# Performance work log

Measured on AMD Instinct MI355X. Metric: run time of the kernel, lower is better.

The kernel has to match this reference:

```python
import jax, jax.numpy as jnp
import numpy as np

P = 32            # patch_num_row
KS = 5            # kernel_size
DIM = 1024
HEADS = 16
DIM_HEAD = 64
INNER = HEADS * DIM_HEAD
SCALE = DIM_HEAD ** -0.5


def _nearby_mask(p=P, ks=KS):
    # True = masked out (matches torch masked_fill semantics)
    pad = ks // 2
    m = np.ones((p * p, p + 2 * pad, p + 2 * pad), dtype=bool)
    for i in range(p):
        for j in range(p):
            m[i * p + j, i:i + ks, j:j + ks] = False
    m = m[:, pad:-pad, pad:-pad].reshape(p * p, p * p)
    # F.pad(mask, (1,0,1,0), value=False): unmasked first row/col (BOS token)
    m = np.pad(m, ((1, 0), (1, 0)), constant_values=False)
    return jnp.asarray(m)  # [n, n], n = p*p + 1

NB_MASK = _nearby_mask()


def setup_inputs() -> dict:
    key = jax.random.key(0)
    ks = jax.random.split(key, 8)
    b, n = 16, P * P + 1
    s = DIM ** -0.5
    return {
        "q": jax.random.normal(ks[0], (b, n, DIM), jnp.float32),
        "k": jax.random.normal(ks[1], (b, n, DIM), jnp.float32),
        "v": jax.random.normal(ks[2], (b, n, DIM), jnp.float32),
        "Wq": jax.random.normal(ks[3], (DIM, INNER), jnp.float32) * s,
        "Wk": jax.random.normal(ks[4], (DIM, INNER), jnp.float32) * s,
        "Wv": jax.random.normal(ks[5], (DIM, INNER), jnp.float32) * s,
        "Wo": jax.random.normal(ks[6], (INNER, DIM), jnp.float32) * (INNER ** -0.5),
        "bo": jnp.zeros((DIM,), jnp.float32),
    }


def reference(q, k, v, Wq, Wk, Wv, Wo, bo):
    b, n, _ = q.shape
    h, d = HEADS, DIM_HEAD
    # projections, split heads: b n (h d) -> b h n d
    qh = (q @ Wq).reshape(b, n, h, d).transpose(0, 2, 1, 3)
    kh = (k @ Wk).reshape(b, n, h, d).transpose(0, 2, 1, 3)
    vh = (v @ Wv).reshape(b, n, h, d).transpose(0, 2, 1, 3)
    dots = jnp.einsum('bhid,bhjd->bhij', qh, kh) * SCALE
    mask_value = -jnp.finfo(dots.dtype).max
    dots = jnp.where(NB_MASK[None, None], mask_value, dots)
    attn = jax.nn.softmax(dots, axis=-1)
    out = jnp.einsum('bhij,bhjd->bhid', attn, vh)
    out = out.transpose(0, 2, 1, 3).reshape(b, n, h * d)
    return out @ Wo + bo
```

## Files before the change

### kernel.cpp

```cpp
#include <hip/hip_runtime.h>

typedef unsigned short u16;
typedef unsigned int   u32;
typedef __attribute__((ext_vector_type(8))) __bf16 bf16x8;
typedef __attribute__((ext_vector_type(4))) float   f32x4;

#define MROWS 16400
#define NPADROWS 16512
#define KD 1024
#define MATEL ((size_t)NPADROWS * KD)
#define NT 32

__device__ __forceinline__ u16 f2b(float f) {
  union { float f; u32 u; } x; x.f = f;
  return (u16)((x.u + 0x7FFFu + ((x.u >> 16) & 1u)) >> 16);
}
__device__ __forceinline__ float b2f(u16 h) {
  union { u32 u; float f; } x; x.u = ((u32)h) << 16;
  return x.f;
}

__device__ __forceinline__ void gll16(const u16* g, u16* l) {
  __builtin_amdgcn_global_load_lds(
      (const __attribute__((address_space(1))) void*)g,
      (__attribute__((address_space(3))) void*)l, 16, 0, 0);
}

__global__ __launch_bounds__(256) void k_pre(
    const float* __restrict__ W0, const float* __restrict__ W1,
    const float* __restrict__ W2, const float* __restrict__ W3,
    u16* __restrict__ T,
    const float* __restrict__ q, const float* __restrict__ k,
    const float* __restrict__ v, u16* __restrict__ dst)
{
  if (blockIdx.x < 4096) {
    __shared__ float tile[32][33];
    int z = blockIdx.x >> 10;
    int tl = blockIdx.x & 1023;
    int k0 = (tl >> 5) * 32, n0 = (tl & 31) * 32;
    int tx = threadIdx.x & 31, ty = threadIdx.x >> 5;
    const float* W = (z == 0) ? W0 : (z == 1) ? W1 : (z == 2) ? W2 : W3;
    u16* Tz = T + (size_t)z * KD * KD;
#pragma unroll
    for (int r = ty; r < 32; r += 8)
      tile[r][tx] = W[(size_t)(k0 + r) * KD + n0 + tx];
    __syncthreads();
#pragma unroll
    for (int r = ty; r < 32; r += 8)
      Tz[(size_t)(n0 + r) * KD + k0 + tx] = f2b(tile[tx][r]);
  } else {
    int cid = blockIdx.x - 4096;
    const size_t CH_PER_MAT = MATEL / 8;
    const size_t total = 3 * CH_PER_MAT;
    for (size_t c = (size_t)cid * 256 + threadIdx.x; c < total;
         c += (size_t)2048 * 256) {
      size_t z = c / CH_PER_MAT;
      size_t r = c - z * CH_PER_MAT;
      size_t row = r >> 7;
      int col8 = (int)(r & 127) * 8;
      u16* o = dst + z * MATEL + row * KD + col8;
      if (row < MROWS) {
        const float* s = ((z == 0) ? q : (z == 1) ? k : v) + row * KD + col8;
        float4 f0 = *(const float4*)s;
        float4 f1 = *(const float4*)(s + 4);
        ushort4 o0; o0.x = f2b(f0.x); o0.y = f2b(f0.y); o0.z = f2b(f0.z); o0.w = f2b(f0.w);
        ushort4 o1; o1.x = f2b(f1.x); o1.y = f2b(f1.y); o1.z = f2b(f1.z); o1.w = f2b(f1.w);
        *(ushort4*)o = o0; *(ushort4*)(o + 4) = o1;
      } else {
        ushort4 zz; zz.x = zz.y = zz.z = zz.w = 0;
        *(ushort4*)o = zz; *(ushort4*)(o + 4) = zz;
      }
    }
  }
}

template<bool OUT_FP32>
__global__ __launch_bounds__(512, 1) void k_gemm256(
    const u16* __restrict__ Ab, const u16* __restrict__ Bt,
    u16* __restrict__ Cb, float* __restrict__ Cf,
    const float* __restrict__ bias, int nwg)
{
  __shared__ u16 lds[3 * 16384];

  int lin = blockIdx.x;
  int qq = nwg >> 3, r8 = nwg & 7;
  int xcd = lin & 7, pos = lin >> 3;
  int wg = (xcd < r8 ? xcd * (qq + 1) : r8 * (qq + 1) + (xcd - r8) * qq) + pos;
  int bn = wg & 3;
  int rest = wg >> 2;
  int bm = rest % 65;
  int z  = rest / 65;

  int t = threadIdx.x;
  int w = t >> 6, l = t & 63;
  int lrow = l & 15, kgrp = l >> 4;
  int wrow = w >> 2, wcol = w & 3;

  int pr = t >> 2;
  int ccl = ((t & 3) ^ ((t >> 3) & 3)) * 8;
  int ar0 = bm * 256 + pr;        if (ar0 > NPADROWS - 1) ar0 = NPADROWS - 1;
  int ar1 = bm * 256 + 128 + pr;  if (ar1 > NPADROWS - 1) ar1 = NPADROWS - 1;
  const u16* gA0 = Ab + (size_t)z * MATEL + (size_t)ar0 * KD + ccl;
  const u16* gA1 = Ab + (size_t)z * MATEL + (size_t)ar1 * KD + ccl;
  const u16* gB0 = Bt + (size_t)z * (1024 * 1024) + (size_t)(bn * 256 + pr) * KD + ccl;
  const u16* gB1 = gB0 + (size_t)128 * KD;

  int qr = (lrow >> 1) & 3;
  int xk = (kgrp ^ qr) * 8;

  f32x4 acc[8][4] = {};
  bf16x8 afr[4], bfr2[2];

#define STAGE(B) { u16* L = lds + (B) * 16384;                          \
    gll16(gA0, L + w * 512);          gll16(gA1, L + 4096 + w * 512);   \
    gll16(gB0, L + 8192 + w * 512);   gll16(gB1, L + 12288 + w * 512);  \
    gA0 += 32; gA1 += 32; gB0 += 32; gB1 += 32; }

#define WAITV4 do { __builtin_amdgcn_sched_barrier(0);                  \
    asm volatile("s_waitcnt vmcnt(4)" ::: "memory");                    \
    __builtin_amdgcn_sched_barrier(0); } while (0)
#define WAITV0 do { __builtin_amdgcn_sched_barrier(0);                  \
    asm volatile("s_waitcnt vmcnt(0)" ::: "memory");                    \
    __builtin_amdgcn_sched_barrier(0); } while (0)
#define BAR do { __builtin_amdgcn_sched_barrier(0);                     \
    __builtin_amdgcn_s_barrier();                                       \
    __builtin_amdgcn_sched_barrier(0); } while (0)

#define READ_A(FM0) {                                                   \
    _Pragma("unroll")                                                   \
    for (int qa = 0; qa < 4; ++qa)                                      \
      afr[qa] = *(const bf16x8*)(Lb + (wrow * 128 + (FM0 + qa) * 16 + lrow) * 32 + xk); }
#define READ_B(FN0) {                                                   \
    _Pragma("unroll")                                                   \
    for (int qb = 0; qb < 2; ++qb)                                      \
      bfr2[qb] = *(const bf16x8*)(Lb + 8192 + (wcol * 64 + (FN0 + qb) * 16 + lrow) * 32 + xk); }
#define MFMA_Q(FM0, FN0) {                                              \
    __builtin_amdgcn_s_setprio(1);                                      \
    _Pragma("unroll")                                                   \
    for (int qa = 0; qa < 4; ++qa)                                      \
      _Pragma("unroll")                                                 \
      for (int qb = 0; qb < 2; ++qb)                                    \
        acc[FM0 + qa][FN0 + qb] = __builtin_amdgcn_mfma_f32_16x16x32_bf16( \
            afr[qa], bfr2[qb], acc[FM0 + qa][FN0 + qb], 0, 0, 0);       \
    __builtin_amdgcn_s_setprio(0); }

  STAGE(0); STAGE(1);
  WAITV4;
  BAR;

  int cur = 0;
  for (int kt = 0; kt < NT; ++kt) {
    if (kt + 2 < NT) {
      int pre = cur + 2; if (pre >= 3) pre -= 3;
      STAGE(pre);
    }
    const u16* Lb = lds + cur * 16384;
    READ_A(0); READ_B(0);
    BAR; MFMA_Q(0, 0); BAR;
    READ_B(2);
    BAR; MFMA_Q(0, 2); BAR;
    READ_A(4);
    BAR; MFMA_Q(4, 2); BAR;
    READ_B(0);
    BAR; MFMA_Q(4, 0);
    if (kt + 1 < NT) {
      if (kt + 2 < NT) { WAITV4; }
      else            { WAITV0; }
      BAR;
    }
    cur += 1; if (cur == 3) cur = 0;
  }
#undef STAGE
#undef WAITV4
#undef WAITV0
#undef BAR
#undef READ_A
#undef READ_B
#undef MFMA_Q

#pragma unroll
  for (int fm = 0; fm < 8; ++fm) {
#pragma unroll
    for (int fn = 0; fn < 4; ++fn) {
      int gcol = bn * 256 + wcol * 64 + fn * 16 + lrow;
#pragma unroll
      for (int r = 0; r < 4; ++r) {
        int grow = bm * 256 + wrow * 128 + fm * 16 + kgrp * 4 + r;
        if constexpr (OUT_FP32) {
          if (grow < MROWS)
            Cf[(size_t)grow * KD + gcol] = acc[fm][fn][r] + bias[gcol];
        } else {
          if (grow < NPADROWS)
            Cb[(size_t)z * MATEL + (size_t)grow * KD + gcol] = f2b(acc[fm][fn][r]);
        }
      }
    }
  }
}

template<bool OUT_FP32>
__global__ __launch_bounds__(256) void k_gemm(
    const u16* __restrict__ Ab, const u16* __restrict__ Bt,
    u16* __restrict__ Cb, float* __restrict__ Cf,
    const float* __restrict__ bias, int nwg)
{
  __shared__ u16 lds[2 * 8192];

  int lin = blockIdx.x;
  int cpx = nwg >> 3;
  int swz = (lin & 7) * cpx + (lin >> 3);
  int bn = swz & 7;
  int rest = swz >> 3;
  int bm = rest % 129;
  int z  = rest / 129;

  int t = threadIdx.x;
  int w = t >> 6, l = t & 63;
  int lrow = l & 15, kgrp = l >> 4;
  int wm = (w >> 1) * 64, wn = (w & 1) * 64;

  int srow = w * 16 + (l >> 2);
  int scol = ((l & 3) ^ ((srow >> 1) & 3)) * 8;
  const u16* gA  = Ab + (size_t)z * MATEL + (size_t)(bm * 128 + srow) * KD + scol;
  const u16* gA2 = gA + (size_t)64 * KD;
  const u16* gB  = Bt + (size_t)z * (1024 * 1024) + (size_t)(bn * 128 + srow) * KD + scol;
  const u16* gB2 = gB + (size_t)64 * KD;
  int dA0 = w * 512;
  int dA1 = 2048 + w * 512;
  int dB0 = 4096 + w * 512;
  int dB1 = 6144 + w * 512;

  int qr = (lrow >> 1) & 3;
  int aoff[4], boff[4];
#pragma unroll
  for (int fm = 0; fm < 4; ++fm)
    aoff[fm] = (wm + fm * 16 + lrow) * 32 + ((kgrp ^ qr) * 8);
#pragma unroll
  for (int fn = 0; fn < 4; ++fn)
    boff[fn] = 4096 + (wn + fn * 16 + lrow) * 32 + ((kgrp ^ qr) * 8);

  f32x4 acc[4][4] = {};

#define STAGE(B) { u16* L = lds + (B) * 8192;                         \
    gll16(gA,  L + dA0); gll16(gA2, L + dA1);                         \
    gll16(gB,  L + dB0); gll16(gB2, L + dB1);                         \
    gA += 32; gA2 += 32; gB += 32; gB2 += 32; }

  STAGE(0);
  __syncthreads();

  int buf = 0;
#pragma unroll 2
  for (int kt = 0; kt < NT; ++kt) {
    if (kt + 1 < NT) STAGE(buf ^ 1);

    const u16* Lb = lds + buf * 8192;
    bf16x8 af[4], bfr[4];
#pragma unroll
    for (int fm = 0; fm < 4; ++fm)
      af[fm] = *(const bf16x8*)(Lb + aoff[fm]);
#pragma unroll
    for (int fn = 0; fn < 4; ++fn)
      bfr[fn] = *(const bf16x8*)(Lb + boff[fn]);
#pragma unroll
    for (int fm = 0; fm < 4; ++fm)
#pragma unroll
      for (int fn = 0; fn < 4; ++fn)
        acc[fm][fn] = __builtin_amdgcn_mfma_f32_16x16x32_bf16(af[fm], bfr[fn], acc[fm][fn], 0, 0, 0);

    __syncthreads();
    buf ^= 1;
  }
#undef STAGE

#pragma unroll
  for (int fm = 0; fm < 4; ++fm) {
#pragma unroll
    for (int fn = 0; fn < 4; ++fn) {
      int gcol = bn * 128 + wn + fn * 16 + lrow;
#pragma unroll
      for (int r = 0; r < 4; ++r) {
        int grow = bm * 128 + wm + fm * 16 + kgrp * 4 + r;
        if constexpr (OUT_FP32) {
          if (grow < MROWS)
            Cf[(size_t)grow * KD + gcol] = acc[fm][fn][r] + bias[gcol];
        } else {
          Cb[(size_t)z * MATEL + (size_t)grow * KD + gcol] = f2b(acc[fm][fn][r]);
        }
      }
    }
  }
}

__global__ __launch_bounds__(256) void k_attn(
    const u16* __restrict__ Qp, const u16* __restrict__ Kp,
    const u16* __restrict__ Vp, u16* __restrict__ AO)
{
  int t = threadIdx.x;

  if (blockIdx.x >= 256) {
    __shared__ float sdp[4][16][37];
    __shared__ int   keys[37];
    __shared__ unsigned long long incm[4];

    int bid = blockIdx.x - 256;
    int b = bid >> 8;
    int tile = bid & 255;
    int pi0 = (tile >> 4) * 2, pj0 = (tile & 15) * 2;
    size_t rowbase = (size_t)b * 1025;

    int iq[4];
#pragma unroll
    for (int qi = 0; qi < 4; ++qi)
      iq[qi] = 1 + (pi0 + (qi >> 1)) * 32 + (pj0 + (qi & 1));

    if (t < 37) {
      if (t < 36) {
        int r = pi0 - 2 + t / 6, c = pj0 - 2 + t % 6;
        keys[t] = (r >= 0 && r < 32 && c >= 0 && c < 32) ? (1 + r * 32 + c) : -1;
      } else {
        keys[36] = 0;
      }
    }
    if (t < 4) {
      int di = t >> 1, dj = t & 1;
      unsigned long long m = 1ull << 36;
      for (int j = 0; j < 36; ++j) {
        int wr = j / 6, wc = j % 6;
        if (wr >= di && wr < di + 5 && wc >= dj && wc < dj + 5) m |= 1ull << j;
      }
      incm[t] = m;
    }

    int e = t & 3;
    int hD = (t >> 2) & 15;
    float qreg[4][16];
#pragma unroll
    for (int qi = 0; qi < 4; ++qi) {
      const u16* qp = Qp + (rowbase + iq[qi]) * 1024 + hD * 64 + e * 16;
      uint4 a0 = *(const uint4*)qp;
      uint4 a1 = *(const uint4*)(qp + 8);
      u32 uu[8] = {a0.x, a0.y, a0.z, a0.w, a1.x, a1.y, a1.z, a1.w};
#pragma unroll
      for (int u = 0; u < 8; ++u) {
        qreg[qi][u * 2]     = __uint_as_float(uu[u] << 16);
        qreg[qi][u * 2 + 1] = __uint_as_float(uu[u] & 0xffff0000u);
      }
    }
    __syncthreads();

#pragma unroll
    for (int p = 0; p < 10; ++p) {
      int idx = p * 64 + (t >> 2);
      int j = idx >> 4; if (j > 36) j = 36;
      int key = keys[j];
      int krow = key < 0 ? 0 : key;
      const u16* kp = Kp + (rowbase + krow) * 1024 + hD * 64 + e * 16;
      uint4 kv0 = *(const uint4*)kp;
      uint4 kv1 = *(const uint4*)(kp + 8);
      float s0 = 0.f, s1 = 0.f, s2 = 0.f, s3 = 0.f;
      u32 uu[8] = {kv0.x, kv0.y, kv0.z, kv0.w, kv1.x, kv1.y, kv1.z, kv1.w};
#pragma unroll
      for (int u = 0; u < 8; ++u) {
        float lo = __uint_as_float(uu[u] << 16);
        float hi = __uint_as_float(uu[u] & 0xffff0000u);
        s0 += qreg[0][u * 2] * lo + qreg[0][u * 2 + 1] * hi;
        s1 += qreg[1][u * 2] * lo + qreg[1][u * 2 + 1] * hi;
        s2 += qreg[2][u * 2] * lo + qreg[2][u * 2 + 1] * hi;
        s3 += qreg[3][u * 2] * lo + qreg[3][u * 2 + 1] * hi;
      }
      s0 += __shfl_xor(s0, 1); s0 += __shfl_xor(s0, 2);
      s1 += __shfl_xor(s1, 1); s1 += __shfl_xor(s1, 2);
      s2 += __shfl_xor(s2, 1); s2 += __shfl_xor(s2, 2);
      s3 += __shfl_xor(s3, 1); s3 += __shfl_xor(s3, 2);
      if (idx < 592) {
        float sv = (e == 0) ? s0 : (e == 1) ? s1 : (e == 2) ? s2 : s3;
        sdp[e][hD][j] = (key >= 0) ? sv * 0.125f : -3.0e38f;
      }
    }
    __syncthreads();

    {
      int row = t >> 2;
      int qi = row >> 4, hh = row & 15;
      unsigned long long inc = incm[qi];
      float dv[10];
      float m = -3.0e38f;
#pragma unroll
      for (int s = 0; s < 10; ++s) {
        int j = e + s * 4;
        float d = -3.0e38f;
        if (j < 37) {
          d = sdp[qi][hh][j];
          if (!((inc >> j) & 1)) d = -3.0e38f;
        }
        dv[s] = d;
        m = fmaxf(m, d);
      }
      m = fmaxf(m, __shfl_xor(m, 1));
      m = fmaxf(m, __shfl_xor(m, 2));
      float sum = 0.f;
      float pv[10];
#pragma unroll
      for (int s = 0; s < 10; ++s) {
        int j = e + s * 4;
        float p = (j < 37) ? __expf(dv[s] - m) : 0.f;
        pv[s] = p; sum += p;
      }
      sum += __shfl_xor(sum, 1);
      sum += __shfl_xor(sum, 2);
      float inv = 1.f / sum;
#pragma unroll
      for (int s = 0; s < 10; ++s) {
        int j = e + s * 4;
        if (j < 37) sdp[qi][hh][j] = pv[s] * inv;
      }
    }
    __syncthreads();

    {
      int h = t >> 4;
      int c0 = t * 4;
      float a[4][4] = {};
#pragma unroll 4
      for (int j = 0; j < 37; ++j) {
        int key = keys[j];
        int krow = key < 0 ? 0 : key;
        ushort4 vv = *(const ushort4*)(Vp + (rowbase + krow) * 1024 + c0);
        float v0 = b2f(vv.x), v1 = b2f(vv.y), v2 = b2f(vv.z), v3 = b2f(vv.w);
#pragma unroll
        for (int qi = 0; qi < 4; ++qi) {
          float p = sdp[qi][h][j];
          a[qi][0] += p * v0; a[qi][1] += p * v1;
          a[qi][2] += p * v2; a[qi][3] += p * v3;
        }
      }
#pragma unroll
      for (int qi = 0; qi < 4; ++qi) {
        ushort4 o;
        o.x = f2b(a[qi][0]); o.y = f2b(a[qi][1]);
        o.z = f2b(a[qi][2]); o.w = f2b(a[qi][3]);
        *(ushort4*)&AO[(rowbase + iq[qi]) * 1024 + c0] = o;
      }
    }
  } else {
    __shared__ float q0[64];
    __shared__ float pr[1025];
    __shared__ float red[256];
    __shared__ float red4[256][4];
    int bid = blockIdx.x;
    int b = bid >> 4, h = bid & 15;
    size_t rowbase = (size_t)b * 1025;

    if (t < 64) q0[t] = b2f(Qp[rowbase * 1024 + h * 64 + t]);
    __syncthreads();

    float lmax = -3.0e38f;
    for (int j = t; j < 1025; j += 256) {
      const u16* kp = Kp + (rowbase + j) * 1024 + h * 64;
      float s = 0.f;
#pragma unroll
      for (int e = 0; e < 64; e += 4) {
        ushort4 kv = *(const ushort4*)(kp + e);
        s += q0[e + 0] * b2f(kv.x) + q0[e + 1] * b2f(kv.y)
           + q0[e + 2] * b2f(kv.z) + q0[e + 3] * b2f(kv.w);
      }
      s *= 0.125f;
      pr[j] = s;
      lmax = fmaxf(lmax, s);
    }
    red[t] = lmax; __syncthreads();
    for (int s = 128; s > 0; s >>= 1) {
      if (t < s) red[t] = fmaxf(red[t], red[t + s]);
      __syncthreads();
    }
    float m = red[0]; __syncthreads();

    float lsum = 0.f;
    for (int j = t; j < 1025; j += 256) {
      float p = __expf(pr[j] - m);
      pr[j] = p; lsum += p;
    }
    red[t] = lsum; __syncthreads();
    for (int s = 128; s > 0; s >>= 1) {
      if (t < s) red[t] += red[t + s];
      __syncthreads();
    }
    float inv = 1.f / red[0]; __syncthreads();

    int g16 = t & 15, grp = t >> 4;
    int c0 = h * 64 + g16 * 4;
    float a0 = 0, a1 = 0, a2 = 0, a3 = 0;
    for (int j = grp; j < 1025; j += 16) {
      float p = pr[j];
      ushort4 vv = *(const ushort4*)(Vp + (rowbase + j) * 1024 + c0);
      a0 += p * b2f(vv.x); a1 += p * b2f(vv.y);
      a2 += p * b2f(vv.z); a3 += p * b2f(vv.w);
    }
    red4[t][0] = a0; red4[t][1] = a1; red4[t][2] = a2; red4[t][3] = a3;
    __syncthreads();
    for (int s = 128; s >= 16; s >>= 1) {
      if (t < s) {
#pragma unroll
        for (int kx = 0; kx < 4; ++kx) red4[t][kx] += red4[t + s][kx];
      }
      __syncthreads();
    }
    if (t < 16) {
      ushort4 o;
      o.x = f2b(red4[t][0] * inv); o.y = f2b(red4[t][1] * inv);
      o.z = f2b(red4[t][2] * inv); o.w = f2b(red4[t][3] * inv);
      *(ushort4*)&AO[rowbase * 1024 + h * 64 + t * 4] = o;
    }
  }
}

extern "C" void kernel_launch(void* const* d_in, const int* in_sizes, int n_in,
                              void* d_out, int out_size, void* d_ws, size_t ws_size,
                              hipStream_t stream) {
  const float* q  = (const float*)d_in[0];
  const float* k  = (const float*)d_in[1];
  const float* v  = (const float*)d_in[2];
  const float* Wq = (const float*)d_in[3];
  const float* Wk = (const float*)d_in[4];
  const float* Wv = (const float*)d_in[5];
  const float* Wo = (const float*)d_in[6];
  const float* bo = (const float*)d_in[7];
  float* out = (float*)d_out;

  u16* wt = (u16*)d_ws;
  u16* qb = wt + (size_t)4 * 1024 * 1024;
  u16* Qp = qb + 3 * MATEL;
  u16* Kp = Qp + MATEL;
  u16* Vp = Kp + MATEL;
  u16* AO = qb;

  k_pre<<<6144, 256, 0, stream>>>(Wq, Wk, Wv, Wo, wt, q, k, v, qb);

  k_gemm256<false><<<780, 512, 0, stream>>>(qb, wt, Qp, nullptr, nullptr, 780);

  k_attn<<<4352, 256, 0, stream>>>(Qp, Kp, Vp, AO);

  k_gemm<true><<<1032, 256, 0, stream>>>(AO, wt + (size_t)3 * 1024 * 1024,
                                         nullptr, out, bo, 1032);
}
```

Baseline: 350.0 us.

## Compute local-window QK scores with MFMA and fuse masked softmax in registers

In the neighbourhood-attention blocks, the scalar per-thread QK dot product is replaced by bf16 16x16x32 MFMA instructions. Each wave handles four heads against 48 padded key slots, and Q/K fragments are loaded straight from global memory. The masked softmax now runs on the MFMA accumulators using cross-lane shuffles, and the normalized probabilities go to shared memory. This removes the separate score and softmax phases and one barrier. In exchange, the 16-row MFMA tile holds only 4 distinct queries, so most of its work is redundant.

```diff
diff --git a/kernel.cpp b/kernel.cpp
--- a/kernel.cpp
+++ b/kernel.cpp
@@ -2,6 +2,7 @@
 
 typedef unsigned short u16;
 typedef unsigned int   u32;
+typedef unsigned long long u64;
 typedef __attribute__((ext_vector_type(8))) __bf16 bf16x8;
 typedef __attribute__((ext_vector_type(4))) float   f32x4;
 
@@ -301,7 +302,7 @@
   if (blockIdx.x >= 256) {
     __shared__ float sdp[4][16][37];
     __shared__ int   keys[37];
-    __shared__ unsigned long long incm[4];
+    __shared__ u64   incm[4];
 
     int bid = blockIdx.x - 256;
     int b = bid >> 8;
@@ -324,96 +325,95 @@
     }
     if (t < 4) {
       int di = t >> 1, dj = t & 1;
-      unsigned long long m = 1ull << 36;
+      u64 m = 1ull << 36;
       for (int j = 0; j < 36; ++j) {
         int wr = j / 6, wc = j % 6;
         if (wr >= di && wr < di + 5 && wc >= dj && wc < dj + 5) m |= 1ull << j;
       }
       incm[t] = m;
     }
-
-    int e = t & 3;
-    int hD = (t >> 2) & 15;
-    float qreg[4][16];
-#pragma unroll
-    for (int qi = 0; qi < 4; ++qi) {
-      const u16* qp = Qp + (rowbase + iq[qi]) * 1024 + hD * 64 + e * 16;
-      uint4 a0 = *(const uint4*)qp;
-      uint4 a1 = *(const uint4*)(qp + 8);
-      u32 uu[8] = {a0.x, a0.y, a0.z, a0.w, a1.x, a1.y, a1.z, a1.w};
-#pragma unroll
-      for (int u = 0; u < 8; ++u) {
-        qreg[qi][u * 2]     = __uint_as_float(uu[u] << 16);
-        qreg[qi][u * 2 + 1] = __uint_as_float(uu[u] & 0xffff0000u);
-      }
-    }
     __syncthreads();
 
-#pragma unroll
-    for (int p = 0; p < 10; ++p) {
-      int idx = p * 64 + (t >> 2);
-      int j = idx >> 4; if (j > 36) j = 36;
-      int key = keys[j];
-      int krow = key < 0 ? 0 : key;
-      const u16* kp = Kp + (rowbase + krow) * 1024 + hD * 64 + e * 16;
-      uint4 kv0 = *(const uint4*)kp;
-      uint4 kv1 = *(const uint4*)(kp + 8);
-      float s0 = 0.f, s1 = 0.f, s2 = 0.f, s3 = 0.f;
-      u32 uu[8] = {kv0.x, kv0.y, kv0.z, kv0.w, kv1.x, kv1.y, kv1.z, kv1.w};
-#pragma unroll
-      for (int u = 0; u < 8; ++u) {
-        float lo = __uint_as_float(uu[u] << 16);
-        float hi = __uint_as_float(uu[u] & 0xffff0000u);
-        s0 += qreg[0][u * 2] * lo + qreg[0][u * 2 + 1] * hi;
-        s1 += qreg[1][u * 2] * lo + qreg[1][u * 2 + 1] * hi;
-        s2 += qreg[2][u * 2] * lo + qreg[2][u * 2 + 1] * hi;
-        s3 += qreg[3][u * 2] * lo + qreg[3][u * 2 + 1] * hi;
-      }
-      s0 += __shfl_xor(s0, 1); s0 += __shfl_xor(s0, 2);
-      s1 += __shfl_xor(s1, 1); s1 += __shfl_xor(s1, 2);
-      s2 += __shfl_xor(s2, 1); s2 += __shfl_xor(s2, 2);
-      s3 += __shfl_xor(s3, 1); s3 += __shfl_xor(s3, 2);
-      if (idx < 592) {
-        float sv = (e == 0) ? s0 : (e == 1) ? s1 : (e == 2) ? s2 : s3;
-        sdp[e][hD][j] = (key >= 0) ? sv * 0.125f : -3.0e38f;
-      }
-    }
-    __syncthreads();
-
     {
-      int row = t >> 2;
-      int qi = row >> 4, hh = row & 15;
-      unsigned long long inc = incm[qi];
-      float dv[10];
-      float m = -3.0e38f;
-#pragma unroll
-      for (int s = 0; s < 10; ++s) {
-        int j = e + s * 4;
-        float d = -3.0e38f;
-        if (j < 37) {
-          d = sdp[qi][hh][j];
-          if (!((inc >> j) & 1)) d = -3.0e38f;
+      int l = t & 63, w = t >> 6;
+      int kap = l & 15, kg = l >> 4;
+
+      int jj0 = kap, jj1 = 16 + kap, jj2 = 32 + kap;
+      int kraw0 = keys[jj0];
+      int kraw1 = keys[jj1];
+      int kraw2 = (jj2 < 37) ? keys[jj2] : -1;
+      int krow0 = kraw0 < 0 ? 0 : kraw0;
+      int krow1 = kraw1 < 0 ? 0 : kraw1;
+      int krow2 = kraw2 < 0 ? 0 : kraw2;
+      int qrow = iq[kap & 3];
+
+      u64 im0 = incm[0], im1 = incm[1], im2 = incm[2], im3 = incm[3];
+
+      const float NEG = -3.0e38f;
+      const size_t qoff = (rowbase + qrow) * 1024 + kg * 8;
+      const size_t k0off = (rowbase + krow0) * 1024 + kg * 8;
+      const size_t k1off = (rowbase + krow1) * 1024 + kg * 8;
+      const size_t k2off = (rowbase + krow2) * 1024 + kg * 8;
+
+#pragma unroll
+      for (int hh = 0; hh < 4; ++hh) {
+        int h = w * 4 + hh;
+        int hb = h * 64;
+        bf16x8 qa0 = *(const bf16x8*)(Qp + qoff + hb);
+        bf16x8 qa1 = *(const bf16x8*)(Qp + qoff + hb + 32);
+        bf16x8 k00 = *(const bf16x8*)(Kp + k0off + hb);
+        bf16x8 k01 = *(const bf16x8*)(Kp + k0off + hb + 32);
+        bf16x8 k10 = *(const bf16x8*)(Kp + k1off + hb);
+        bf16x8 k11 = *(const bf16x8*)(Kp + k1off + hb + 32);
+        bf16x8 k20 = *(const bf16x8*)(Kp + k2off + hb);
+        bf16x8 k21 = *(const bf16x8*)(Kp + k2off + hb + 32);
+
+        f32x4 c0 = {}, c1 = {}, c2 = {};
+        c0 = __builtin_amdgcn_mfma_f32_16x16x32_bf16(qa0, k00, c0, 0, 0, 0);
+        c0 = __builtin_amdgcn_mfma_f32_16x16x32_bf16(qa1, k01, c0, 0, 0, 0);
+        c1 = __builtin_amdgcn_mfma_f32_16x16x32_bf16(qa0, k10, c1, 0, 0, 0);
+        c1 = __builtin_amdgcn_mfma_f32_16x16x32_bf16(qa1, k11, c1, 0, 0, 0);
+        c2 = __builtin_amdgcn_mfma_f32_16x16x32_bf16(qa0, k20, c2, 0, 0, 0);
+        c2 = __builtin_amdgcn_mfma_f32_16x16x32_bf16(qa1, k21, c2, 0, 0, 0);
+
+        float x0[4], x1[4], x2[4];
+#pragma unroll
+        for (int r = 0; r < 4; ++r) {
+          u64 im = (r == 0) ? im0 : (r == 1) ? im1 : (r == 2) ? im2 : im3;
+          bool ok0 = (kraw0 >= 0) && ((im >> jj0) & 1);
+          bool ok1 = (kraw1 >= 0) && ((im >> jj1) & 1);
+          bool ok2 = (jj2 < 37) && (kraw2 >= 0) && ((im >> jj2) & 1);
+          x0[r] = ok0 ? c0[r] * 0.125f : NEG;
+          x1[r] = ok1 ? c1[r] * 0.125f : NEG;
+          x2[r] = ok2 ? c2[r] * 0.125f : NEG;
         }
-        dv[s] = d;
-        m = fmaxf(m, d);
-      }
-      m = fmaxf(m, __shfl_xor(m, 1));
-      m = fmaxf(m, __shfl_xor(m, 2));
-      float sum = 0.f;
-      float pv[10];
-#pragma unroll
-      for (int s = 0; s < 10; ++s) {
-        int j = e + s * 4;
-        float p = (j < 37) ? __expf(dv[s] - m) : 0.f;
-        pv[s] = p; sum += p;
-      }
-      sum += __shfl_xor(sum, 1);
-      sum += __shfl_xor(sum, 2);
-      float inv = 1.f / sum;
-#pragma unroll
-      for (int s = 0; s < 10; ++s) {
-        int j = e + s * 4;
-        if (j < 37) sdp[qi][hh][j] = pv[s] * inv;
+        float pm0[4], pm1[4], pm2[4], inv[4];
+#pragma unroll
+        for (int r = 0; r < 4; ++r) {
+          float m = fmaxf(fmaxf(x0[r], x1[r]), x2[r]);
+          m = fmaxf(m, __shfl_xor(m, 1));
+          m = fmaxf(m, __shfl_xor(m, 2));
+          m = fmaxf(m, __shfl_xor(m, 4));
+          m = fmaxf(m, __shfl_xor(m, 8));
+          float p0 = __expf(x0[r] - m);
+          float p1 = __expf(x1[r] - m);
+          float p2 = __expf(x2[r] - m);
+          float s = p0 + p1 + p2;
+          s += __shfl_xor(s, 1);
+          s += __shfl_xor(s, 2);
+          s += __shfl_xor(s, 4);
+          s += __shfl_xor(s, 8);
+          pm0[r] = p0; pm1[r] = p1; pm2[r] = p2;
+          inv[r] = 1.f / s;
+        }
+        if (l < 16) {
+#pragma unroll
+          for (int r = 0; r < 4; ++r) {
+            sdp[r][h][jj0] = pm0[r] * inv[r];
+            sdp[r][h][jj1] = pm1[r] * inv[r];
+            if (jj2 < 37) sdp[r][h][jj2] = pm2[r] * inv[r];
+          }
+        }
       }
     }
     __syncthreads();
```

Measured after the change: 359.7 us. 2.8% more time.
